# Optimization experiments

Measured on AMD Instinct MI355X. Metric: run time of the kernel, lower is better.

Reference implementation:

```python
import jax, jax.numpy as jnp
import numpy as np

B, C, H, W = 2, 64, 128, 128
HEADS, DH = 8, 32
DN = ('NCHW', 'OIHW', 'NCHW')


def _conv(x, w, pad):
    return jax.lax.conv_general_dilated(x, w, (1, 1), [(pad, pad), (pad, pad)], dimension_numbers=DN)


def _rconv3(x, w):
    # Conv3x3 module: ReflectionPad2d(1) then 3x3 VALID conv, no bias
    xp = jnp.pad(x, ((0, 0), (0, 0), (1, 1), (1, 1)), mode='reflect')
    return jax.lax.conv_general_dilated(xp, w, (1, 1), 'VALID', dimension_numbers=DN)


def _prelu(x, a):
    return jnp.where(x > 0, x, a * x)


def _l2n(x):
    # F.normalize(p=2, dim=-1), eps=1e-12
    return x / jnp.maximum(jnp.linalg.norm(x, axis=-1, keepdims=True), 1e-12)


def _ln(y, g, b):
    mu = y.mean(-1, keepdims=True)
    v = ((y - mu) ** 2).mean(-1, keepdims=True)
    return (y - mu) / jnp.sqrt(v + 1e-5) * g + b


def _qco(x, w1, sw, sb, t1w, t1b, t2w, t2b):
    # QCO_C with level_num == C
    b, Cc = x.shape[0], x.shape[1]
    L = Cc
    x1 = _rconv3(x, w1)
    x_ave = _conv(jnp.mean(x1, (2, 3), keepdims=True), sw, 0) + sb[None, :, None, None]  # [b,C,1,1]
    xq = x_ave.reshape(b, Cc)
    mn = xq.min(-1, keepdims=True)
    mx = xq.max(-1, keepdims=True)
    qs = jnp.arange(L, dtype=x.dtype)
    ql = (2.0 * qs + 1.0) / (2.0 * L) * (mx - mn) + mn  # [b,L]
    inter = (ql[:, 1] - ql[:, 0])[:, None, None]  # [b,1,1]
    quant = 1.0 - jnp.abs(ql[:, None, :] - xq[:, :, None])  # [b,C,L]
    quant = quant * (quant > 1.0 - inter)
    sta = quant.sum(1)  # [b,L]
    sta = sta / sta.sum(-1, keepdims=True)
    out = jnp.concatenate([sta[:, :, None, None], x_ave], axis=1)  # [b,2C,1,1]
    out = jax.nn.relu(_conv(out, t1w, 0) + t1b[None, :, None, None])
    out = jax.nn.relu(_conv(out, t2w, 0) + t2b[None, :, None, None])
    return out  # [b,C,1,1]


def _attention(x, w_down, w_mid, w_up, wq_l, wk_m, wv_m, wq_h, rescale,
               w_proj_l, b_proj_l, w_proj_h, b_proj_h,
               qco_w1, qco_sca_w, qco_sca_b, qco_t1_w, qco_t1_b, qco_t2_w, qco_t2_b,
               rsp_w1, rsp_prelu, rsp_w2, c31_w1, c31_prelu, c31_w2, c31_w3):
    b, Cc, Hh, Ww = x.shape
    n = Hh * Ww
    # QKV conv projections (Conv2d, zero pad 1, no bias)
    xCL = jnp.moveaxis(_conv(x, w_down, 1), 1, -1)  # [b,h,w,C]
    xCM = jnp.moveaxis(_conv(x, w_mid, 1), 1, -1)   # [b,h,w,2C]
    xCH = jnp.moveaxis(_conv(x, w_up, 1), 1, -1)    # [b,h,w,3C]
    xL = xCL.reshape(b, n, Cc)
    xM = xCM.reshape(b, n, 2 * Cc)
    xH = xCH.reshape(b, n, 3 * Cc)

    def to_heads(t, d):  # [b,n,heads*d] -> [b,heads,d,n]
        return t.reshape(b, n, HEADS, d).transpose(0, 2, 3, 1)

    q_l = _l2n(to_heads(xL @ wq_l.T, DH))            # [b,heads,DH,n]
    k_m = _l2n(to_heads(xM @ wk_m.T, 2 * DH))        # [b,heads,2DH,n]
    v_m = to_heads(xM @ wv_m.T, 2 * DH)              # [b,heads,2DH,n]
    q_h = _l2n(to_heads(xH @ wq_h.T, 3 * DH))        # [b,heads,3DH,n]

    attn_l = jax.nn.softmax(jnp.einsum('bhdn,bhen->bhde', q_l, k_m) * rescale, axis=-1)  # [b,heads,DH,2DH]
    attn_h = jax.nn.softmax(jnp.einsum('bhdn,bhen->bhde', q_h, k_m) * rescale, axis=-1)  # [b,heads,3DH,2DH]

    x_l = jnp.einsum('bhde,bhen->bhdn', attn_l, v_m).transpose(0, 3, 1, 2).reshape(b, n, HEADS * DH)
    x_h = jnp.einsum('bhde,bhen->bhdn', attn_h, v_m).transpose(0, 3, 1, 2).reshape(b, n, HEADS * 3 * DH)
    # NOTE: torch code does .view(b, c, h, w) on [b, n, c] output -> raw memory reinterpretation,
    # which is exactly jnp.reshape here (faithful to the original, including this quirk).
    out_cl = (x_l @ w_proj_l.T + b_proj_l).reshape(b, Cc, Hh, Ww)
    out_ch = (x_h @ w_proj_h.T + b_proj_h).reshape(b, 3 * Cc, Hh, Ww)

    Hcat = jnp.concatenate([out_cl, out_ch], axis=1)  # [b,4C,h,w]
    H_out = _rconv3(_prelu(_rconv3(Hcat, rsp_w1), rsp_prelu), rsp_w2)  # ReshapeBlock -> [b,C,h,w]
    att_before = _qco(jnp.moveaxis(xCL, -1, 1), qco_w1, qco_sca_w, qco_sca_b,
                      qco_t1_w, qco_t1_b, qco_t2_w, qco_t2_b)  # [b,C,1,1]
    t = _prelu(_rconv3(H_out, c31_w1), c31_prelu)
    H_add = _conv(_rconv3(t, c31_w2), c31_w3, 0)  # Conv3_1
    return H_add + H_out * att_before


def _ff_block(z, g, bb, w1, b1, w2, b2):
    # PreNorm(LayerNorm over channel) + FeedForward(Linear, LeakyReLU(0.01), Linear)
    y = jnp.moveaxis(z, 1, -1)
    y = _ln(y, g, bb)
    y = y @ w1.T + b1
    y = jnp.where(y > 0, y, 0.01 * y)
    y = y @ w2.T + b2
    return jnp.moveaxis(y, -1, 1)


def _forward(x, w_down, w_mid, w_up, wq_l, wk_m, wv_m, wq_h, rescale,
             w_proj_l, b_proj_l, w_proj_h, b_proj_h,
             qco_w1, qco_sca_w, qco_sca_b, qco_t1_w, qco_t1_b, qco_t2_w, qco_t2_b,
             rsp_w1, rsp_prelu, rsp_w2, c31_w1, c31_prelu, c31_w2, c31_w3,
             ln1_g, ln1_b, ff1_w1, ff1_b1, ff1_w2, ff1_b2,
             ln2_g, ln2_b, ff2_w1, ff2_b1, ff2_w2, ff2_b2):
    out1 = _attention(x, w_down, w_mid, w_up, wq_l, wk_m, wv_m, wq_h, rescale,
                      w_proj_l, b_proj_l, w_proj_h, b_proj_h,
                      qco_w1, qco_sca_w, qco_sca_b, qco_t1_w, qco_t1_b, qco_t2_w, qco_t2_b,
                      rsp_w1, rsp_prelu, rsp_w2, c31_w1, c31_prelu, c31_w2, c31_w3) + x
    out2 = _ff_block(out1, ln1_g, ln1_b, ff1_w1, ff1_b1, ff1_w2, ff1_b2) + out1
    out3 = _ff_block(out2, ln2_g, ln2_b, ff2_w1, ff2_b1, ff2_w2, ff2_b2) + out1
    return out3


def setup_inputs() -> dict:
    keys = iter(jax.random.split(jax.random.key(0), 48))

    def rn(shape, s=0.05):
        return (jax.random.normal(next(keys), shape, jnp.float32) * s)

    d = {
        'x': rn((B, C, H, W), 1.0),
        'w_down': rn((C, C, 3, 3)), 'w_mid': rn((2 * C, C, 3, 3)), 'w_up': rn((3 * C, C, 3, 3)),
        'wq_l': rn((HEADS * DH, C)), 'wk_m': rn((2 * HEADS * DH, 2 * C)),
        'wv_m': rn((2 * HEADS * DH, 2 * C)), 'wq_h': rn((3 * HEADS * DH, 3 * C)),
        'rescale': jnp.ones((HEADS, 1, 1), jnp.float32),
        'w_proj_l': rn((C, HEADS * DH)), 'b_proj_l': rn((C,)),
        'w_proj_h': rn((3 * C, 3 * HEADS * DH)), 'b_proj_h': rn((3 * C,)),
        'qco_w1': rn((C, C, 3, 3)), 'qco_sca_w': rn((C, C, 1, 1)), 'qco_sca_b': rn((C,)),
        'qco_t1_w': rn((C, 2 * C, 1, 1)), 'qco_t1_b': rn((C,)),
        'qco_t2_w': rn((C, C, 1, 1)), 'qco_t2_b': rn((C,)),
        'rsp_w1': rn((C, 4 * C, 3, 3)), 'rsp_prelu': jnp.array(0.25, jnp.float32), 'rsp_w2': rn((C, C, 3, 3)),
        'c31_w1': rn((C, C, 3, 3)), 'c31_prelu': jnp.array(0.25, jnp.float32),
        'c31_w2': rn((C, C, 3, 3)), 'c31_w3': rn((C, C, 1, 1)),
        'ln1_g': jnp.ones((C,), jnp.float32), 'ln1_b': jnp.zeros((C,), jnp.float32),
        'ff1_w1': rn((C, C)), 'ff1_b1': rn((C,)), 'ff1_w2': rn((C, C)), 'ff1_b2': rn((C,)),
        'ln2_g': jnp.ones((C,), jnp.float32), 'ln2_b': jnp.zeros((C,), jnp.float32),
        'ff2_w1': rn((C, C)), 'ff2_b1': rn((C,)), 'ff2_w2': rn((C, C)), 'ff2_b2': rn((C,)),
    }
    return d


def reference(x, w_down, w_mid, w_up, wq_l, wk_m, wv_m, wq_h, rescale,
              w_proj_l, b_proj_l, w_proj_h, b_proj_h,
              qco_w1, qco_sca_w, qco_sca_b, qco_t1_w, qco_t1_b, qco_t2_w, qco_t2_b,
              rsp_w1, rsp_prelu, rsp_w2, c31_w1, c31_prelu, c31_w2, c31_w3,
              ln1_g, ln1_b, ff1_w1, ff1_b1, ff1_w2, ff1_b2,
              ln2_g, ln2_b, ff2_w1, ff2_b1, ff2_w2, ff2_b2):
    return _forward(x, w_down, w_mid, w_up, wq_l, wk_m, wv_m, wq_h, rescale,
                    w_proj_l, b_proj_l, w_proj_h, b_proj_h,
                    qco_w1, qco_sca_w, qco_sca_b, qco_t1_w, qco_t1_b, qco_t2_w, qco_t2_b,
                    rsp_w1, rsp_prelu, rsp_w2, c31_w1, c31_prelu, c31_w2, c31_w3,
                    ln1_g, ln1_b, ff1_w1, ff1_b1, ff1_w2, ff1_b2,
                    ln2_g, ln2_b, ff2_w1, ff2_b1, ff2_w2, ff2_b2)
```

## Files before the change

kernel.cpp:

```cpp
#include <hip/hip_runtime.h>
#include <hip/hip_bf16.h>
#include <stdint.h>

typedef __hip_bfloat16 bf16;
typedef __attribute__((ext_vector_type(8))) __bf16 bf8v;
typedef __attribute__((ext_vector_type(8))) short short8;
typedef __attribute__((ext_vector_type(4))) short short4v;
typedef __attribute__((ext_vector_type(4))) float f32x4;
#define DEVINL __device__ __forceinline__
#define MFMA16(a,b,c) __builtin_amdgcn_mfma_f32_16x16x32_bf16((a),(b),(c),0,0,0)

DEVINL short f2bs(float f) { bf16 h = __float2bfloat16(f); return *reinterpret_cast<short*>(&h); }
DEVINL float bs2f(short s) { bf16 h = *reinterpret_cast<bf16*>(&s); return __bfloat162float(h); }


static const size_t OFF_ZBF   = 0;
static const size_t OFF_WTQ   = 29360128;
static const size_t OFF_WTR1  = 29802496;
static const size_t OFF_WTR2  = 30097408;
static const size_t OFF_WTC1  = 30171136;
static const size_t OFF_WTF   = 30244864;
static const size_t OFF_W1T   = 30318592;
static const size_t OFF_SCAWT = 30466048;
static const size_t OFF_T1WT  = 30482432;
static const size_t OFF_T2WT  = 30515200;
static const size_t OFF_GB    = 31645696;
static const size_t OFF_WQLB  = 32235520;
static const size_t OFF_WKMB  = 32268288;
static const size_t OFF_WQHB  = 32399360;
static const size_t OFF_T1    = 41082880;
static const size_t OFF_UL    = 41345024;
static const size_t OFF_UK    = 41476096;
static const size_t OFF_T1H   = 42000384;
static const size_t OFF_UH    = 42786816;
static const size_t OFF_NORMS = 43966464;
static const size_t OFF_ATTL  = 43978752;
static const size_t OFF_ATTH  = 44109824;
static const size_t OFF_WEL   = 44503040;
static const size_t OFF_WEH   = 44765184;
static const size_t OFF_ACATB = 45813760;
static const size_t OFF_TSUM  = 45944832;
static const size_t OFF_ATTB  = 45949440;
static const size_t OFF_HCATB = 45949952;
static const size_t OFF_MIDB  = 62727168;
static const size_t OFF_HOUTB = 66921472;
static const size_t OFF_WFFB  = 71115776;
static const size_t OFF_GPART = 79504384;
static const size_t OFF_HCATT = 79504384;
static const size_t OFF_XT    = 98378752;
static const size_t WS_BYTES  = 102573056;

__global__ __launch_bounds__(256) void k_transp(const float* __restrict__ x,
                                                short* __restrict__ xt) {
  __shared__ short sT[64][72];
  const int t = threadIdx.x, b = blockIdx.z, p0 = blockIdx.x * 64;
  for (int i = t; i < 1024; i += 256) {
    int c = i >> 4, p4 = (i & 15) * 4;
    float4 g = *(const float4*)&x[(((size_t)(b * 64 + c)) << 14) + p0 + p4];
    sT[p4 + 0][c] = f2bs(g.x);
    sT[p4 + 1][c] = f2bs(g.y);
    sT[p4 + 2][c] = f2bs(g.z);
    sT[p4 + 3][c] = f2bs(g.w);
  }
  __syncthreads();
  for (int i = t; i < 512; i += 256) {
    int p = i >> 3, co = (i & 7) * 8;
    *(short8*)&xt[((((size_t)b << 14) + p0 + p)) * 64 + co] = *(short8*)&sT[p][co];
  }
}

__global__ __launch_bounds__(256) void k_transph(const short* __restrict__ hc,
                                                 short* __restrict__ ht) {
  __shared__ short sT[64][72];
  const int t = threadIdx.x, b = blockIdx.z, p0 = blockIdx.x * 64, c0 = blockIdx.y * 64;
  for (int i = t; i < 512; i += 256) {
    int c = i >> 3, qo = (i & 7) * 8;
    short8 v = *(const short8*)&hc[(((size_t)(b * 256 + c0 + c)) << 14) + p0 + qo];
#pragma unroll
    for (int u = 0; u < 8; u++) sT[qo + u][c] = v[u];
  }
  __syncthreads();
  for (int i = t; i < 512; i += 256) {
    int q = i >> 3, co = (i & 7) * 8;
    *(short8*)&ht[((size_t)(b * 16384 + p0 + q)) * 256 + c0 + co] = *(short8*)&sT[q][co];
  }
}

__global__ void k_prep_all(const float* __restrict__ wd, const float* __restrict__ wm,
                           const float* __restrict__ wu, const float* __restrict__ rw1,
                           const float* __restrict__ rw2, const float* __restrict__ cw1,
                           const float* __restrict__ wql, const float* __restrict__ wkm,
                           const float* __restrict__ wqh,
                           const float* __restrict__ c31w3, const float* __restrict__ c31w2,
                           const float* __restrict__ qw1, const float* __restrict__ qscaw,
                           const float* __restrict__ qt1w, const float* __restrict__ qt2w,
                           const float* __restrict__ f11, const float* __restrict__ f12,
                           const float* __restrict__ f21, const float* __restrict__ f22,
                           bf16* __restrict__ wtq, bf16* __restrict__ wtr1,
                           bf16* __restrict__ wtr2, bf16* __restrict__ wtc1,
                           bf16* __restrict__ wqlb, bf16* __restrict__ wkmb,
                           bf16* __restrict__ wqhb, bf16* __restrict__ wtf,
                           float* __restrict__ w1t, float* __restrict__ scawt,
                           float* __restrict__ t1wt, float* __restrict__ t2wt,
                           bf16* __restrict__ wffb) {
  int i = blockIdx.x * 256 + threadIdx.x;
  if (i < 221184) {
    int tap = i / 24576, r = i % 24576, oc = r >> 6, ic = r & 63;
    float v;
    if (oc < 64)       v = wd[(oc * 64 + ic) * 9 + tap];
    else if (oc < 192) v = wm[((oc - 64) * 64 + ic) * 9 + tap];
    else               v = wu[((oc - 192) * 64 + ic) * 9 + tap];
    wtq[i] = __float2bfloat16(v);
  } else if (i < 368640) {
    int j = i - 221184;
    int tap = j / 16384, r = j % 16384, oc = r >> 8, ic = r & 255;
    wtr1[j] = __float2bfloat16(rw1[(oc * 256 + ic) * 9 + tap]);
  } else if (i < 405504) {
    int j = i - 368640;
    int tap = j / 4096, r = j % 4096, oc = r >> 6, ic = r & 63;
    wtr2[j] = __float2bfloat16(rw2[(oc * 64 + ic) * 9 + tap]);
// ... 26 lines not shown
    int o = i - 749568;
    int c = o & 63, jj = o >> 6;
    t1wt[o] = qt1w[c * 128 + jj];
  } else if (i < 761856) {
    int o = i - 757760;
    int c = o & 63, jj = o >> 6;
    t2wt[o] = qt2w[c * 64 + jj];
  } else if (i < 778240) {
    int j = i - 761856;
    int stage = j >> 12, r = j & 4095;
    const float* src = (stage == 0) ? f11 : (stage == 1) ? f12 : (stage == 2) ? f21 : f22;
    wffb[j] = __float2bfloat16(src[r]);
  }
}

__global__ __launch_bounds__(256) void k_convq(
    const short* __restrict__ xt, const short* __restrict__ wtq,
    bf16* __restrict__ zbf)
{
  __shared__ short sX[3][130][72];
  const int t = threadIdx.x, lane = t & 63, wv = t >> 6;
  const int y = blockIdx.x, ocg = blockIdx.y, b = blockIdx.z;

  for (int i = t; i < 3120; i += 256) {
    int ko = i & 7, c2 = i >> 3, col = c2 % 130, row = c2 / 130;
    int gy = y + row - 1, gx = col - 1;
    short8 vv;
    if ((gy >= 0) & (gy < 128) & (gx >= 0) & (gx < 128)) {
      vv = *(const short8*)&xt[((size_t)b * 1048576 + (size_t)((gy << 7) + gx) * 64) + ko * 8];
    } else {
// ... 310 lines not shown
  float* gp = Gp + ((size_t)(kc * 2 + b)) * 147456;
#pragma unroll
  for (int m = 0; m < 2; m++)
#pragma unroll
    for (int n = 0; n < 2; n++)
#pragma unroll
      for (int r = 0; r < 4; r++) {
        const int row = ti * 64 + wo * 32 + m * 16 + ((lane >> 4) << 2) + r;
        const int col = tj * 64 + wp * 32 + n * 16 + (lane & 15);
        float v = acc[m][n][r];
        gp[(size_t)row * 384 + col] = v;
        if (ti != tj) gp[(size_t)col * 384 + row] = v;
      }
}

__global__ void k_gredb(const float* __restrict__ Gp, bf16* __restrict__ Gb) {
  int i = blockIdx.x * 256 + threadIdx.x;
  if (i >= 294912) return;
  int b = i / 147456, e = i % 147456;
  float s = 0.f;
#pragma unroll
  for (int c = 0; c < 16; c++) s += Gp[(size_t)(c * 2 + b) * 147456 + e];
  Gb[(size_t)b * 147456 + e] = __float2bfloat16(s);
}

struct MJobs5 {
  const short* A[5];
  float* C[5];
  int lda[5], K[5], r0[5], c0[5], ldc[5];
  long sC[5];
  int nx[5], b0[6];
};

__global__ __launch_bounds__(256) void k_mgemm5(MJobs5 J, const short* __restrict__ Gb) {
  const int bx = blockIdx.x, z = blockIdx.y;
  int j = 0;
  while (bx >= J.b0[j + 1]) j++;
  const int local = bx - J.b0[j];
// ... 95 lines not shown
  const float* Bp = J.B[j] + (size_t)z * J.sB[j];
  const int K = J.K[j], lda = J.lda[j];
  const int m = y * 16 + ty, n = x * 16 + tx;
  float acc = 0.f;
  for (int k0 = 0; k0 < K; k0 += 16) {
    sa[ty][tx] = Ap[(size_t)m * lda + k0 + tx];
    sb[ty][tx] = Bp[(size_t)(k0 + ty) * 128 + n];
    __syncthreads();
#pragma unroll
    for (int kk = 0; kk < 16; kk++) acc = fmaf(sa[ty][kk], sb[kk][tx], acc);
    __syncthreads();
  }
  Cb[(size_t)z * 32768 + J.co[j] + (size_t)m * 128 + n] = __float2bfloat16(acc);
}

__global__ __launch_bounds__(256) void k_norms2(
    const float* __restrict__ UL, const float* __restrict__ UK,
    const float* __restrict__ UH,
    const float* __restrict__ wql, const float* __restrict__ wkm,
    const float* __restrict__ wqh, float* __restrict__ norms) {
  const int t = threadIdx.x, lane = t & 63;
  const int row = blockIdx.x * 4 + (t >> 6);
  const int b = row >= 1536 ? 1 : 0;
  const int r = row - b * 1536;
  const float* u; const float* wv; int K;
  if (r < 256)      { K = 64;  u = UL + (size_t)(b * 256 + r) * 64;          wv = wql + (size_t)r * 64; }
  else if (r < 768) { int e = r - 256; K = 128; u = UK + (size_t)(b * 512 + e) * 128; wv = wkm + (size_t)e * 128; }
  else              { int d = r - 768; K = 192; u = UH + (size_t)(b * 768 + d) * 192; wv = wqh + (size_t)d * 192; }
  float s = 0.f;
  for (int k = lane; k < K; k += 64) s = fmaf(u[k], wv[k], s);
#pragma unroll
  for (int o = 32; o; o >>= 1) s += __shfl_xor(s, o);
  if (lane == 0) norms[b * 1536 + r] = fmaxf(sqrtf(fmaxf(s, 0.f)), 1e-12f);
}

__global__ __launch_bounds__(256) void k_attn(
    const float* __restrict__ T1, const float* __restrict__ T1H,
    const float* __restrict__ wkm, const float* __restrict__ norms,
    const float* __restrict__ rescale,
    float* __restrict__ attL, float* __restrict__ attH)
{
  const int h = blockIdx.x, cy = blockIdx.y, b = blockIdx.z;
  const int t = threadIdx.x;
  __shared__ float sK[64 * 129];
  __shared__ float sQ[32 * 129];
  __shared__ float sNk[64];
  const int isL = (cy == 0);
  const int rbase = isL ? 0 : (cy - 1) * 32;
  const float* TQ = isL ? (T1 + (size_t)(b * 256 + h * 32) * 128)
                        : (T1H + (size_t)(b * 768 + h * 96 + rbase) * 128);
  for (int idx = t; idx < 8192; idx += 256) {
    int e = idx >> 7, k = idx & 127;
    sK[e * 129 + k] = wkm[(size_t)(h * 64 + e) * 128 + k];
  }
  for (int idx = t; idx < 4096; idx += 256) {
    int r = idx >> 7, k = idx & 127;
    sQ[r * 129 + k] = TQ[(size_t)r * 128 + k];
  }
  if (t < 64) sNk[t] = norms[b * 1536 + 256 + h * 64 + t];
  __syncthreads();

  const int w = t >> 6, lane = t & 63;
  const float rs = rescale[h];
  for (int r = w; r < 32; r += 4) {
    float s = 0.f;
    for (int k = 0; k < 128; k++) s = fmaf(sQ[r * 129 + k], sK[lane * 129 + k], s);
    float nq = norms[b * 1536 + (isL ? (h * 32 + r) : (768 + h * 96 + rbase + r))];
    float logit = s / (nq * sNk[lane]) * rs;
    float m = logit;
#pragma unroll
    for (int o = 32; o; o >>= 1) m = fmaxf(m, __shfl_xor(m, o));
    float p = __expf(logit - m);
    float den = p;
#pragma unroll
    for (int o = 32; o; o >>= 1) den += __shfl_xor(den, o);
    float av = p / den;
    if (isL) attL[((size_t)(b * 8 + h) * 32 + r) * 64 + lane] = av;
    else     attH[((size_t)(b * 8 + h) * 96 + rbase + r) * 64 + lane] = av;
  }
}

__global__ __launch_bounds__(256) void k_weff(
    const float* __restrict__ attL, const float* __restrict__ attH,
    const float* __restrict__ wvm,
    float* __restrict__ WeL, float* __restrict__ WeH)
{
  const int h = blockIdx.x, br = blockIdx.y, b = blockIdx.z;
  const int M = br ? 96 : 32;
  __shared__ float sAt[96 * 64];
  __shared__ float sV[64 * 132];
  const int t = threadIdx.x;
  const float* asrc = br ? attH + (size_t)(b * 8 + h) * 96 * 64
                         : attL + (size_t)(b * 8 + h) * 32 * 64;
  for (int idx = t; idx < M * 64; idx += 256) sAt[idx] = asrc[idx];
  for (int idx = t; idx < 8192; idx += 256) {
    int e = idx >> 7, k = idx & 127;
    sV[e * 132 + k] = wvm[(size_t)(h * 64 + e) * 128 + k];
  }
  __syncthreads();
  const int jg = t & 31, rw = t >> 5;
  float* dst = br ? WeH + (size_t)(b * 768 + h * 96) * 128
                  : WeL + (size_t)(b * 256 + h * 32) * 128;
  for (int r = rw; r < M; r += 8) {
    float4 acc = make_float4(0.f, 0.f, 0.f, 0.f);
    for (int e = 0; e < 64; e++) {
      float a = sAt[r * 64 + e];
      float4 v4 = *(const float4*)&sV[e * 132 + jg * 4];
      acc.x = fmaf(a, v4.x, acc.x);
      acc.y = fmaf(a, v4.y, acc.y);
      acc.z = fmaf(a, v4.z, acc.z);
      acc.w = fmaf(a, v4.w, acc.w);
    }
    *(float4*)&dst[(size_t)r * 128 + jg * 4] = acc;
  }
}

__global__ __launch_bounds__(256) void k_tsum2(const bf16* __restrict__ Z,
                                               float* __restrict__ Tsum) {
  const int c = blockIdx.x & 63, b = blockIdx.x >> 6;
  const bf16* src = Z + (((size_t)(b * 384 + c)) << 14);
  const int t = threadIdx.x;
  __shared__ float sc[16];
  __shared__ float red[4][9];
  float a9[9] = {};
  for (int i = t; i < 2048; i += 256) {
    int y = i >> 4, x0 = (i & 15) * 8;
    short8 v8 = *(const short8*)&src[(y << 7) + x0];
    float vs[8], s8 = 0.f;
#pragma unroll
    for (int u = 0; u < 8; u++) { vs[u] = bs2f(v8[u]); s8 += vs[u]; }
    a9[0] += s8;
    int ri = (y == 0) ? 0 : (y == 1) ? 1 : (y == 126) ? 2 : (y == 127) ? 3 : -1;
    if (ri >= 0) a9[1 + ri] += s8;
    if (x0 == 0)   { a9[5] += vs[0]; a9[6] += vs[1]; }
    if (x0 == 120) { a9[7] += vs[6]; a9[8] += vs[7]; }
    if (ri >= 0) {
      if (x0 == 0)   { sc[ri * 4 + 0] = vs[0]; sc[ri * 4 + 1] = vs[1]; }
      if (x0 == 120) { sc[ri * 4 + 2] = vs[6]; sc[ri * 4 + 3] = vs[7]; }
    }
  }
#pragma unroll
  for (int q = 0; q < 9; q++)
#pragma unroll
    for (int o = 32; o; o >>= 1) a9[q] += __shfl_xor(a9[q], o);
  const int w = t >> 6;
  if ((t & 63) == 0)
#pragma unroll
    for (int q = 0; q < 9; q++) red[w][q] = a9[q];
  __syncthreads();
  if (t == 0) {
    float s9[9];
#pragma unroll
    for (int q = 0; q < 9; q++) s9[q] = red[0][q] + red[1][q] + red[2][q] + red[3][q];
    const float T = s9[0];
    float R[4] = {s9[1], s9[2], s9[3], s9[4]};
    const float C0 = s9[5], C1 = s9[6], C126 = s9[7], C127 = s9[8];
    float rs[4][3];
#pragma unroll
    for (int ri = 0; ri < 4; ri++) {
      rs[ri][0] = R[ri] - sc[ri * 4 + 3] + sc[ri * 4 + 1];
      rs[ri][1] = R[ri];
      rs[ri][2] = R[ri] - sc[ri * 4 + 0] + sc[ri * 4 + 2];
    }
    float A3[3] = {T - C127 + C1, T, T - C0 + C126};
#pragma unroll
    for (int dx = 0; dx < 3; dx++) {
      Tsum[blockIdx.x * 9 + 0 * 3 + dx] = A3[dx] - rs[3][dx] + rs[1][dx];
      Tsum[blockIdx.x * 9 + 1 * 3 + dx] = A3[dx];
      Tsum[blockIdx.x * 9 + 2 * 3 + dx] = A3[dx] - rs[0][dx] + rs[2][dx];
    }
  }
}

__global__ __launch_bounds__(64) void k_qco(
    const float* __restrict__ Tsum, const float* __restrict__ w1t,
    const float* __restrict__ scawt, const float* __restrict__ scab,
    const float* __restrict__ t1wt, const float* __restrict__ t1b,
    const float* __restrict__ t2wt, const float* __restrict__ t2b,
    float* __restrict__ attb)
{
  const int b = blockIdx.x, c = threadIdx.x;
  __shared__ float sm[64], sxq[64], scat[128], sh1[64];
  float acc = 0.f;
  for (int j = 0; j < 64; j++) {
#pragma unroll
    for (int tap = 0; tap < 9; tap++)
      acc = fmaf(w1t[((j * 9 + tap) << 6) + c], Tsum[(b * 64 + j) * 9 + tap], acc);
  }
  sm[c] = acc * (1.f / 16384.f);
  __syncthreads();
  float xa = scab[c];
  for (int j = 0; j < 64; j++) xa = fmaf(scawt[(j << 6) + c], sm[j], xa);
  sxq[c] = xa;
  __syncthreads();
  float mn = xa, mx = xa;
#pragma unroll
  for (int o = 32; o; o >>= 1) {
    mn = fminf(mn, __shfl_xor(mn, o));
    mx = fmaxf(mx, __shfl_xor(mx, o));
  }
  float inter = (mx - mn) * (1.f / 64.f);
  float ql = (2.f * c + 1.f) / 128.f * (mx - mn) + mn;
  float sta = 0.f;
  for (int j = 0; j < 64; j++) {
    float q = 1.f - fabsf(ql - sxq[j]);
    sta += (q > 1.f - inter) ? q : 0.f;
  }
  float tot = sta;
#pragma unroll
  for (int o = 32; o; o >>= 1) tot += __shfl_xor(tot, o);
  sta = sta / fmaxf(tot, 1e-30f);
  scat[c] = sta; scat[64 + c] = xa;
  __syncthreads();
  float h = t1b[c];
  for (int j = 0; j < 128; j++) h = fmaf(t1wt[(j << 6) + c], scat[j], h);
  h = fmaxf(h, 0.f);
  sh1[c] = h;
  __syncthreads();
  float o2 = t2b[c];
  for (int j = 0; j < 64; j++) o2 = fmaf(t2wt[(j << 6) + c], sh1[j], o2);
  attb[b * 64 + c] = fmaxf(o2, 0.f);
}

extern "C" void kernel_launch(void* const* d_in, const int* in_sizes, int n_in,
                              void* d_out, int out_size, void* d_ws, size_t ws_size,
                              hipStream_t stream)
{
  if (ws_size < WS_BYTES) return;
  char* ws = (char*)d_ws;

  const float* x       = (const float*)d_in[0];
  const float* w_down  = (const float*)d_in[1];
  const float* w_mid   = (const float*)d_in[2];
  const float* w_up    = (const float*)d_in[3];
  const float* wq_l    = (const float*)d_in[4];
  const float* wk_m    = (const float*)d_in[5];
// ... 40 lines not shown
  float* w1t   = (float*)(ws + OFF_W1T);
  float* scawt = (float*)(ws + OFF_SCAWT);
  float* t1wt  = (float*)(ws + OFF_T1WT);
  float* t2wt  = (float*)(ws + OFF_T2WT);
  bf16*  Gb    = (bf16*)(ws + OFF_GB);
  bf16*  wqlb  = (bf16*)(ws + OFF_WQLB);
  bf16*  wkmb  = (bf16*)(ws + OFF_WKMB);
  bf16*  wqhb  = (bf16*)(ws + OFF_WQHB);
  float* gpart = (float*)(ws + OFF_GPART);
  float* T1    = (float*)(ws + OFF_T1);
  float* UL    = (float*)(ws + OFF_UL);
  float* UK    = (float*)(ws + OFF_UK);
  float* T1H   = (float*)(ws + OFF_T1H);
  float* UH    = (float*)(ws + OFF_UH);
  float* norms = (float*)(ws + OFF_NORMS);
  float* attL  = (float*)(ws + OFF_ATTL);
  float* attH  = (float*)(ws + OFF_ATTH);
  float* WeL   = (float*)(ws + OFF_WEL);
  float* WeH   = (float*)(ws + OFF_WEH);
  bf16*  acatb = (bf16*)(ws + OFF_ACATB);
  float* tsum  = (float*)(ws + OFF_TSUM);
  float* attb  = (float*)(ws + OFF_ATTB);
  bf16*  hcatb = (bf16*)(ws + OFF_HCATB);
  short* hcatT = (short*)(ws + OFF_HCATT);
  short* midb  = (short*)(ws + OFF_MIDB);
  short* houtb = (short*)(ws + OFF_HOUTB);
  bf16*  wffb  = (bf16*)(ws + OFF_WFFB);
  short* xt    = (short*)(ws + OFF_XT);

  k_transp<<<dim3(256, 1, 2), 256, 0, stream>>>(x, xt);
  k_prep_all<<<dim3(3040), 256, 0, stream>>>(
      w_down, w_mid, w_up, rsp_w1, rsp_w2, c31_w1, wq_l, wk_m, wq_h,
      c31_w3, c31_w2, qco_w1, qsca_w, qt1_w, qt2_w,
      ff1_w1, ff1_w2, ff2_w1, ff2_w2,
      wtq, wtr1, wtr2, wtc1, wqlb, wkmb, wqhb, wtf,
      w1t, scawt, t1wt, t2wt, wffb);

  k_convq<<<dim3(128, 2, 2), 256, 0, stream>>>(xt, (const short*)wtq, zbf);

  k_gramm<<<dim3(21, 16, 2), 256, 0, stream>>>((const short*)zbf, gpart);
  k_gredb<<<dim3(1152), 256, 0, stream>>>(gpart, Gb);

  k_tsum2<<<dim3(128), 256, 0, stream>>>(zbf, tsum);

  MJobs5 M5;
  M5.A[0] = (const short*)wqlb; M5.lda[0] = 64;  M5.K[0] = 64;  M5.r0[0] = 0;   M5.c0[0] = 64;  M5.C[0] = T1;  M5.ldc[0] = 128; M5.sC[0] = 32768;  M5.nx[0] = 2;
  M5.A[1] = (const short*)wqlb; M5.lda[1] = 64;  M5.K[1] = 64;  M5.r0[1] = 0;   M5.c0[1] = 0;   M5.C[1] = UL;  M5.ldc[1] = 64;  M5.sC[1] = 16384;  M5.nx[1] = 1;
  M5.A[2] = (const short*)wkmb; M5.lda[2] = 128; M5.K[2] = 128; M5.r0[2] = 64;  M5.c0[2] = 64;  M5.C[2] = UK;  M5.ldc[2] = 128; M5.sC[2] = 65536;  M5.nx[2] = 2;
  M5.A[3] = (const short*)wqhb; M5.lda[3] = 192; M5.K[3] = 192; M5.r0[3] = 192; M5.c0[3] = 64;  M5.C[3] = T1H; M5.ldc[3] = 128; M5.sC[3] = 98304;  M5.nx[3] = 2;
  M5.A[4] = (const short*)wqhb; M5.lda[4] = 192; M5.K[4] = 192; M5.r0[4] = 192; M5.c0[4] = 192; M5.C[4] = UH;  M5.ldc[4] = 192; M5.sC[4] = 147456; M5.nx[4] = 3;
  M5.b0[0] = 0; M5.b0[1] = 8; M5.b0[2] = 12; M5.b0[3] = 28; M5.b0[4] = 52; M5.b0[5] = 88;
  k_mgemm5<<<dim3(88, 2), 256, 0, stream>>>(M5, (const short*)Gb);

  k_norms2<<<dim3(768), 256, 0, stream>>>(UL, UK, UH, wq_l, wk_m, wq_h, norms);
  k_qco<<<dim3(2), 64, 0, stream>>>(tsum, w1t, scawt, qsca_b, t1wt, qt1_b, t2wt, qt2_b, attb);
  k_attn<<<dim3(8, 4, 2), 256, 0, stream>>>(T1, T1H, wk_m, norms, rescale, attL, attH);
  k_weff<<<dim3(8, 2, 2), 256, 0, stream>>>(attL, attH, wv_m, WeL, WeH);

  Jobs2 J2;
  J2.A[0] = w_proj_l; J2.B[0] = WeL; J2.K[0] = 256; J2.lda[0] = 256; J2.sB[0] = 32768; J2.nx[0] = 8; J2.co[0] = 0;
  J2.A[1] = w_proj_h; J2.B[1] = WeH; J2.K[1] = 768; J2.lda[1] = 768; J2.sB[1] = 98304; J2.nx[1] = 8; J2.co[1] = 8192;
  J2.b0[0] = 0; J2.b0[1] = 32; J2.b0[2] = 128;
  k_sgemm2b<<<dim3(128, 2), 256, 0, stream>>>(J2, acatb);

  k_pixm<<<dim3(256, 4, 2), 256, 0, stream>>>((const short*)zbf, (const short*)acatb,
                                              b_proj_l, b_proj_h, hcatb);

  k_transph<<<dim3(256, 4, 2), 256, 0, stream>>>((const short*)hcatb, hcatT);

  k_conv64<1><<<dim3(128, 2, 2), 256, 0, stream>>>(
      hcatT, 256, 4194304L, 256, (const short*)wtr1, midb, rsp_pr);
  k_conv64<0><<<dim3(128, 2, 2), 256, 0, stream>>>(
// ... 11 lines not shown
```

Before: 271.5 us.

## Merge small independent kernels and fuse attention softmax with value-weight product

Folds the input transpose into the weight-prep launch and the Gram reduction and tile-sum into one launch (`k_gt`). It also puts the norms and QCO head in one launch (`k_nq`) and fuses attention logits/softmax with the effective-weight product in `k_attw`, keeping attention probabilities in shared memory. This removes several kernel launches and the global round trip for attL/attH. The trade-off is that the fused attention kernel runs only 16 blocks, handling both branches serially with large shared-memory use, so there is less parallelism for that stage.

```diff
diff --git a/kernel.cpp b/kernel.cpp
--- a/kernel.cpp
+++ b/kernel.cpp
@@ -34,8 +34,6 @@
 static const size_t OFF_T1H   = 42000384;
 static const size_t OFF_UH    = 42786816;
 static const size_t OFF_NORMS = 43966464;
-static const size_t OFF_ATTL  = 43978752;
-static const size_t OFF_ATTH  = 44109824;
 static const size_t OFF_WEL   = 44503040;
 static const size_t OFF_WEH   = 44765184;
 static const size_t OFF_ACATB = 45813760;
@@ -50,60 +48,46 @@
 static const size_t OFF_XT    = 98378752;
 static const size_t WS_BYTES  = 102573056;
 
-__global__ __launch_bounds__(256) void k_transp(const float* __restrict__ x,
-                                                short* __restrict__ xt) {
+__global__ __launch_bounds__(256) void k_prep_all(
+    const float* __restrict__ wd, const float* __restrict__ wm,
+    const float* __restrict__ wu, const float* __restrict__ rw1,
+    const float* __restrict__ rw2, const float* __restrict__ cw1,
+    const float* __restrict__ wql, const float* __restrict__ wkm,
+    const float* __restrict__ wqh,
+    const float* __restrict__ c31w3, const float* __restrict__ c31w2,
+    const float* __restrict__ qw1, const float* __restrict__ qscaw,
+    const float* __restrict__ qt1w, const float* __restrict__ qt2w,
+    const float* __restrict__ f11, const float* __restrict__ f12,
+    const float* __restrict__ f21, const float* __restrict__ f22,
+    const float* __restrict__ x,
+    bf16* __restrict__ wtq, bf16* __restrict__ wtr1,
+    bf16* __restrict__ wtr2, bf16* __restrict__ wtc1,
+    bf16* __restrict__ wqlb, bf16* __restrict__ wkmb,
+    bf16* __restrict__ wqhb, bf16* __restrict__ wtf,
+    float* __restrict__ w1t, float* __restrict__ scawt,
+    float* __restrict__ t1wt, float* __restrict__ t2wt,
+    bf16* __restrict__ wffb, short* __restrict__ xt) {
   __shared__ short sT[64][72];
-  const int t = threadIdx.x, b = blockIdx.z, p0 = blockIdx.x * 64;
-  for (int i = t; i < 1024; i += 256) {
-    int c = i >> 4, p4 = (i & 15) * 4;
-    float4 g = *(const float4*)&x[(((size_t)(b * 64 + c)) << 14) + p0 + p4];
-    sT[p4 + 0][c] = f2bs(g.x);
-    sT[p4 + 1][c] = f2bs(g.y);
-    sT[p4 + 2][c] = f2bs(g.z);
-    sT[p4 + 3][c] = f2bs(g.w);
-  }
-  __syncthreads();
-  for (int i = t; i < 512; i += 256) {
-    int p = i >> 3, co = (i & 7) * 8;
-    *(short8*)&xt[((((size_t)b << 14) + p0 + p)) * 64 + co] = *(short8*)&sT[p][co];
-  }
-}
-
-__global__ __launch_bounds__(256) void k_transph(const short* __restrict__ hc,
-                                                 short* __restrict__ ht) {
-  __shared__ short sT[64][72];
-  const int t = threadIdx.x, b = blockIdx.z, p0 = blockIdx.x * 64, c0 = blockIdx.y * 64;
-  for (int i = t; i < 512; i += 256) {
-    int c = i >> 3, qo = (i & 7) * 8;
-    short8 v = *(const short8*)&hc[(((size_t)(b * 256 + c0 + c)) << 14) + p0 + qo];
-#pragma unroll
-    for (int u = 0; u < 8; u++) sT[qo + u][c] = v[u];
-  }
-  __syncthreads();
-  for (int i = t; i < 512; i += 256) {
-    int q = i >> 3, co = (i & 7) * 8;
-    *(short8*)&ht[((size_t)(b * 16384 + p0 + q)) * 256 + c0 + co] = *(short8*)&sT[q][co];
-  }
-}
-
-__global__ void k_prep_all(const float* __restrict__ wd, const float* __restrict__ wm,
-                           const float* __restrict__ wu, const float* __restrict__ rw1,
-                           const float* __restrict__ rw2, const float* __restrict__ cw1,
-                           const float* __restrict__ wql, const float* __restrict__ wkm,
-                           const float* __restrict__ wqh,
-                           const float* __restrict__ c31w3, const float* __restrict__ c31w2,
-                           const float* __restrict__ qw1, const float* __restrict__ qscaw,
-                           const float* __restrict__ qt1w, const float* __restrict__ qt2w,
-                           const float* __restrict__ f11, const float* __restrict__ f12,
-                           const float* __restrict__ f21, const float* __restrict__ f22,
-                           bf16* __restrict__ wtq, bf16* __restrict__ wtr1,
-                           bf16* __restrict__ wtr2, bf16* __restrict__ wtc1,
-                           bf16* __restrict__ wqlb, bf16* __restrict__ wkmb,
-                           bf16* __restrict__ wqhb, bf16* __restrict__ wtf,
-                           float* __restrict__ w1t, float* __restrict__ scawt,
-                           float* __restrict__ t1wt, float* __restrict__ t2wt,
-                           bf16* __restrict__ wffb) {
-  int i = blockIdx.x * 256 + threadIdx.x;
+  const int t = threadIdx.x;
+  if (blockIdx.x >= 3040) {
+    const int j = blockIdx.x - 3040;
+    const int b = j >> 8, p0 = (j & 255) * 64;
+    for (int i = t; i < 1024; i += 256) {
+      int c = i >> 4, p4 = (i & 15) * 4;
+      float4 g = *(const float4*)&x[(((size_t)(b * 64 + c)) << 14) + p0 + p4];
+      sT[p4 + 0][c] = f2bs(g.x);
+      sT[p4 + 1][c] = f2bs(g.y);
+      sT[p4 + 2][c] = f2bs(g.z);
+      sT[p4 + 3][c] = f2bs(g.w);
+    }
+    __syncthreads();
+    for (int i = t; i < 512; i += 256) {
+      int p = i >> 3, co = (i & 7) * 8;
+      *(short8*)&xt[((((size_t)b << 14) + p0 + p)) * 64 + co] = *(short8*)&sT[p][co];
+    }
+    return;
+  }
+  int i = blockIdx.x * 256 + t;
   if (i < 221184) {
     int tap = i / 24576, r = i % 24576, oc = r >> 6, ic = r & 63;
     float v;
@@ -160,6 +144,23 @@
   }
 }
 
+__global__ __launch_bounds__(256) void k_transph(const short* __restrict__ hc,
+                                                 short* __restrict__ ht) {
+  __shared__ short sT[64][72];
+  const int t = threadIdx.x, b = blockIdx.z, p0 = blockIdx.x * 64, c0 = blockIdx.y * 64;
+  for (int i = t; i < 512; i += 256) {
+    int c = i >> 3, qo = (i & 7) * 8;
+    short8 v = *(const short8*)&hc[(((size_t)(b * 256 + c0 + c)) << 14) + p0 + qo];
+#pragma unroll
+    for (int u = 0; u < 8; u++) sT[qo + u][c] = v[u];
+  }
+  __syncthreads();
+  for (int i = t; i < 512; i += 256) {
+    int q = i >> 3, co = (i & 7) * 8;
+    *(short8*)&ht[((size_t)(b * 16384 + p0 + q)) * 256 + c0 + co] = *(short8*)&sT[q][co];
+  }
+}
+
 __global__ __launch_bounds__(256) void k_convq(
     const short* __restrict__ xt, const short* __restrict__ wtq,
     bf16* __restrict__ zbf)
@@ -500,14 +501,74 @@
       }
 }
 
-__global__ void k_gredb(const float* __restrict__ Gp, bf16* __restrict__ Gb) {
-  int i = blockIdx.x * 256 + threadIdx.x;
-  if (i >= 294912) return;
-  int b = i / 147456, e = i % 147456;
-  float s = 0.f;
-#pragma unroll
-  for (int c = 0; c < 16; c++) s += Gp[(size_t)(c * 2 + b) * 147456 + e];
-  Gb[(size_t)b * 147456 + e] = __float2bfloat16(s);
+__global__ __launch_bounds__(256) void k_gt(const float* __restrict__ Gp,
+                                            bf16* __restrict__ Gb,
+                                            const bf16* __restrict__ Z,
+                                            float* __restrict__ Tsum) {
+  __shared__ float sc[16];
+  __shared__ float red[4][9];
+  const int t = threadIdx.x;
+  if (blockIdx.x < 1152) {
+    int i = blockIdx.x * 256 + t;
+    if (i >= 294912) return;
+    int b = i / 147456, e = i % 147456;
+    float s = 0.f;
+#pragma unroll
+    for (int c = 0; c < 16; c++) s += Gp[(size_t)(c * 2 + b) * 147456 + e];
+    Gb[(size_t)b * 147456 + e] = __float2bfloat16(s);
+    return;
+  }
+  const int bid = blockIdx.x - 1152;
+  const int c = bid & 63, b = bid >> 6;
+  const bf16* src = Z + (((size_t)(b * 384 + c)) << 14);
+  float a9[9] = {};
+  for (int i = t; i < 2048; i += 256) {
+    int y = i >> 4, x0 = (i & 15) * 8;
+    short8 v8 = *(const short8*)&src[(y << 7) + x0];
+    float vs[8], s8 = 0.f;
+#pragma unroll
+    for (int u = 0; u < 8; u++) { vs[u] = bs2f(v8[u]); s8 += vs[u]; }
+    a9[0] += s8;
+    int ri = (y == 0) ? 0 : (y == 1) ? 1 : (y == 126) ? 2 : (y == 127) ? 3 : -1;
+    if (ri >= 0) a9[1 + ri] += s8;
+    if (x0 == 0)   { a9[5] += vs[0]; a9[6] += vs[1]; }
+    if (x0 == 120) { a9[7] += vs[6]; a9[8] += vs[7]; }
+    if (ri >= 0) {
+      if (x0 == 0)   { sc[ri * 4 + 0] = vs[0]; sc[ri * 4 + 1] = vs[1]; }
+      if (x0 == 120) { sc[ri * 4 + 2] = vs[6]; sc[ri * 4 + 3] = vs[7]; }
+    }
+  }
+#pragma unroll
+  for (int q = 0; q < 9; q++)
+#pragma unroll
+    for (int o = 32; o; o >>= 1) a9[q] += __shfl_xor(a9[q], o);
+  const int w = t >> 6;
+  if ((t & 63) == 0)
+#pragma unroll
+    for (int q = 0; q < 9; q++) red[w][q] = a9[q];
+  __syncthreads();
+  if (t == 0) {
+    float s9[9];
+#pragma unroll
+    for (int q = 0; q < 9; q++) s9[q] = red[0][q] + red[1][q] + red[2][q] + red[3][q];
+    const float T = s9[0];
+    float R[4] = {s9[1], s9[2], s9[3], s9[4]};
+    const float C0 = s9[5], C1 = s9[6], C126 = s9[7], C127 = s9[8];
+    float rs[4][3];
+#pragma unroll
+    for (int ri = 0; ri < 4; ri++) {
+      rs[ri][0] = R[ri] - sc[ri * 4 + 3] + sc[ri * 4 + 1];
+      rs[ri][1] = R[ri];
+      rs[ri][2] = R[ri] - sc[ri * 4 + 0] + sc[ri * 4 + 2];
+    }
+    float A3[3] = {T - C127 + C1, T, T - C0 + C126};
+#pragma unroll
+    for (int dx = 0; dx < 3; dx++) {
+      Tsum[bid * 9 + 0 * 3 + dx] = A3[dx] - rs[3][dx] + rs[1][dx];
+      Tsum[bid * 9 + 1 * 3 + dx] = A3[dx];
+      Tsum[bid * 9 + 2 * 3 + dx] = A3[dx] - rs[0][dx] + rs[2][dx];
+    }
+  }
 }
 
 struct MJobs5 {
@@ -633,212 +694,150 @@
   Cb[(size_t)z * 32768 + J.co[j] + (size_t)m * 128 + n] = __float2bfloat16(acc);
 }
 
-__global__ __launch_bounds__(256) void k_norms2(
+__global__ __launch_bounds__(256) void k_nq(
     const float* __restrict__ UL, const float* __restrict__ UK,
     const float* __restrict__ UH,
     const float* __restrict__ wql, const float* __restrict__ wkm,
-    const float* __restrict__ wqh, float* __restrict__ norms) {
-  const int t = threadIdx.x, lane = t & 63;
-  const int row = blockIdx.x * 4 + (t >> 6);
-  const int b = row >= 1536 ? 1 : 0;
-  const int r = row - b * 1536;
-  const float* u; const float* wv; int K;
-  if (r < 256)      { K = 64;  u = UL + (size_t)(b * 256 + r) * 64;          wv = wql + (size_t)r * 64; }
-  else if (r < 768) { int e = r - 256; K = 128; u = UK + (size_t)(b * 512 + e) * 128; wv = wkm + (size_t)e * 128; }
-  else              { int d = r - 768; K = 192; u = UH + (size_t)(b * 768 + d) * 192; wv = wqh + (size_t)d * 192; }
-  float s = 0.f;
-  for (int k = lane; k < K; k += 64) s = fmaf(u[k], wv[k], s);
-#pragma unroll
-  for (int o = 32; o; o >>= 1) s += __shfl_xor(s, o);
-  if (lane == 0) norms[b * 1536 + r] = fmaxf(sqrtf(fmaxf(s, 0.f)), 1e-12f);
-}
-
-__global__ __launch_bounds__(256) void k_attn(
-    const float* __restrict__ T1, const float* __restrict__ T1H,
-    const float* __restrict__ wkm, const float* __restrict__ norms,
-    const float* __restrict__ rescale,
-    float* __restrict__ attL, float* __restrict__ attH)
-{
-  const int h = blockIdx.x, cy = blockIdx.y, b = blockIdx.z;
-  const int t = threadIdx.x;
-  __shared__ float sK[64 * 129];
-  __shared__ float sQ[32 * 129];
-  __shared__ float sNk[64];
-  const int isL = (cy == 0);
-  const int rbase = isL ? 0 : (cy - 1) * 32;
-  const float* TQ = isL ? (T1 + (size_t)(b * 256 + h * 32) * 128)
-                        : (T1H + (size_t)(b * 768 + h * 96 + rbase) * 128);
-  for (int idx = t; idx < 8192; idx += 256) {
-    int e = idx >> 7, k = idx & 127;
-    sK[e * 129 + k] = wkm[(size_t)(h * 64 + e) * 128 + k];
-  }
-  for (int idx = t; idx < 4096; idx += 256) {
-    int r = idx >> 7, k = idx & 127;
-    sQ[r * 129 + k] = TQ[(size_t)r * 128 + k];
-  }
-  if (t < 64) sNk[t] = norms[b * 1536 + 256 + h * 64 + t];
-  __syncthreads();
-
-  const int w = t >> 6, lane = t & 63;
-  const float rs = rescale[h];
-  for (int r = w; r < 32; r += 4) {
-    float s = 0.f;
-    for (int k = 0; k < 128; k++) s = fmaf(sQ[r * 129 + k], sK[lane * 129 + k], s);
-    float nq = norms[b * 1536 + (isL ? (h * 32 + r) : (768 + h * 96 + rbase + r))];
-    float logit = s / (nq * sNk[lane]) * rs;
-    float m = logit;
-#pragma unroll
-    for (int o = 32; o; o >>= 1) m = fmaxf(m, __shfl_xor(m, o));
-    float p = __expf(logit - m);
-    float den = p;
-#pragma unroll
-    for (int o = 32; o; o >>= 1) den += __shfl_xor(den, o);
-    float av = p / den;
-    if (isL) attL[((size_t)(b * 8 + h) * 32 + r) * 64 + lane] = av;
-    else     attH[((size_t)(b * 8 + h) * 96 + rbase + r) * 64 + lane] = av;
-  }
-}
-
-__global__ __launch_bounds__(256) void k_weff(
-    const float* __restrict__ attL, const float* __restrict__ attH,
-    const float* __restrict__ wvm,
-    float* __restrict__ WeL, float* __restrict__ WeH)
-{
-  const int h = blockIdx.x, br = blockIdx.y, b = blockIdx.z;
-  const int M = br ? 96 : 32;
-  __shared__ float sAt[96 * 64];
-  __shared__ float sV[64 * 132];
-  const int t = threadIdx.x;
-  const float* asrc = br ? attH + (size_t)(b * 8 + h) * 96 * 64
-                         : attL + (size_t)(b * 8 + h) * 32 * 64;
-  for (int idx = t; idx < M * 64; idx += 256) sAt[idx] = asrc[idx];
-  for (int idx = t; idx < 8192; idx += 256) {
-    int e = idx >> 7, k = idx & 127;
-    sV[e * 132 + k] = wvm[(size_t)(h * 64 + e) * 128 + k];
-  }
-  __syncthreads();
-  const int jg = t & 31, rw = t >> 5;
-  float* dst = br ? WeH + (size_t)(b * 768 + h * 96) * 128
-                  : WeL + (size_t)(b * 256 + h * 32) * 128;
-  for (int r = rw; r < M; r += 8) {
-    float4 acc = make_float4(0.f, 0.f, 0.f, 0.f);
-    for (int e = 0; e < 64; e++) {
-      float a = sAt[r * 64 + e];
-      float4 v4 = *(const float4*)&sV[e * 132 + jg * 4];
-      acc.x = fmaf(a, v4.x, acc.x);
-      acc.y = fmaf(a, v4.y, acc.y);
-      acc.z = fmaf(a, v4.z, acc.z);
-      acc.w = fmaf(a, v4.w, acc.w);
-    }
-    *(float4*)&dst[(size_t)r * 128 + jg * 4] = acc;
-  }
-}
-
-__global__ __launch_bounds__(256) void k_tsum2(const bf16* __restrict__ Z,
-                                               float* __restrict__ Tsum) {
-  const int c = blockIdx.x & 63, b = blockIdx.x >> 6;
-  const bf16* src = Z + (((size_t)(b * 384 + c)) << 14);
-  const int t = threadIdx.x;
-  __shared__ float sc[16];
-  __shared__ float red[4][9];
-  float a9[9] = {};
-  for (int i = t; i < 2048; i += 256) {
-    int y = i >> 4, x0 = (i & 15) * 8;
-    short8 v8 = *(const short8*)&src[(y << 7) + x0];
-    float vs[8], s8 = 0.f;
-#pragma unroll
-    for (int u = 0; u < 8; u++) { vs[u] = bs2f(v8[u]); s8 += vs[u]; }
-    a9[0] += s8;
-    int ri = (y == 0) ? 0 : (y == 1) ? 1 : (y == 126) ? 2 : (y == 127) ? 3 : -1;
-    if (ri >= 0) a9[1 + ri] += s8;
-    if (x0 == 0)   { a9[5] += vs[0]; a9[6] += vs[1]; }
-    if (x0 == 120) { a9[7] += vs[6]; a9[8] += vs[7]; }
-    if (ri >= 0) {
-      if (x0 == 0)   { sc[ri * 4 + 0] = vs[0]; sc[ri * 4 + 1] = vs[1]; }
-      if (x0 == 120) { sc[ri * 4 + 2] = vs[6]; sc[ri * 4 + 3] = vs[7]; }
-    }
-  }
-#pragma unroll
-  for (int q = 0; q < 9; q++)
-#pragma unroll
-    for (int o = 32; o; o >>= 1) a9[q] += __shfl_xor(a9[q], o);
-  const int w = t >> 6;
-  if ((t & 63) == 0)
-#pragma unroll
-    for (int q = 0; q < 9; q++) red[w][q] = a9[q];
-  __syncthreads();
-  if (t == 0) {
-    float s9[9];
-#pragma unroll
-    for (int q = 0; q < 9; q++) s9[q] = red[0][q] + red[1][q] + red[2][q] + red[3][q];
-    const float T = s9[0];
-    float R[4] = {s9[1], s9[2], s9[3], s9[4]};
-    const float C0 = s9[5], C1 = s9[6], C126 = s9[7], C127 = s9[8];
-    float rs[4][3];
-#pragma unroll
-    for (int ri = 0; ri < 4; ri++) {
-      rs[ri][0] = R[ri] - sc[ri * 4 + 3] + sc[ri * 4 + 1];
-      rs[ri][1] = R[ri];
-      rs[ri][2] = R[ri] - sc[ri * 4 + 0] + sc[ri * 4 + 2];
-    }
-    float A3[3] = {T - C127 + C1, T, T - C0 + C126};
-#pragma unroll
-    for (int dx = 0; dx < 3; dx++) {
-      Tsum[blockIdx.x * 9 + 0 * 3 + dx] = A3[dx] - rs[3][dx] + rs[1][dx];
-      Tsum[blockIdx.x * 9 + 1 * 3 + dx] = A3[dx];
-      Tsum[blockIdx.x * 9 + 2 * 3 + dx] = A3[dx] - rs[0][dx] + rs[2][dx];
-    }
-  }
-}
-
-__global__ __launch_bounds__(64) void k_qco(
+    const float* __restrict__ wqh, float* __restrict__ norms,
     const float* __restrict__ Tsum, const float* __restrict__ w1t,
     const float* __restrict__ scawt, const float* __restrict__ scab,
     const float* __restrict__ t1wt, const float* __restrict__ t1b,
     const float* __restrict__ t2wt, const float* __restrict__ t2b,
     float* __restrict__ attb)
 {
-  const int b = blockIdx.x, c = threadIdx.x;
   __shared__ float sm[64], sxq[64], scat[128], sh1[64];
-  float acc = 0.f;
-  for (int j = 0; j < 64; j++) {
-#pragma unroll
-    for (int tap = 0; tap < 9; tap++)
-      acc = fmaf(w1t[((j * 9 + tap) << 6) + c], Tsum[(b * 64 + j) * 9 + tap], acc);
-  }
-  sm[c] = acc * (1.f / 16384.f);
+  const int t = threadIdx.x, lane = t & 63;
+  if (blockIdx.x < 768) {
+    const int row = blockIdx.x * 4 + (t >> 6);
+    const int b = row >= 1536 ? 1 : 0;
+    const int r = row - b * 1536;
+    const float* u; const float* wv; int K;
+    if (r < 256)      { K = 64;  u = UL + (size_t)(b * 256 + r) * 64;          wv = wql + (size_t)r * 64; }
+    else if (r < 768) { int e = r - 256; K = 128; u = UK + (size_t)(b * 512 + e) * 128; wv = wkm + (size_t)e * 128; }
+    else              { int d = r - 768; K = 192; u = UH + (size_t)(b * 768 + d) * 192; wv = wqh + (size_t)d * 192; }
+    float s = 0.f;
+    for (int k = lane; k < K; k += 64) s = fmaf(u[k], wv[k], s);
+#pragma unroll
+    for (int o = 32; o; o >>= 1) s += __shfl_xor(s, o);
+    if (lane == 0) norms[b * 1536 + r] = fmaxf(sqrtf(fmaxf(s, 0.f)), 1e-12f);
+    return;
+  }
+  const int b = blockIdx.x - 768, c = t;
+  if (t < 64) {
+    float acc = 0.f;
+    for (int j = 0; j < 64; j++) {
+#pragma unroll
+      for (int tap = 0; tap < 9; tap++)
+        acc = fmaf(w1t[((j * 9 + tap) << 6) + c], Tsum[(b * 64 + j) * 9 + tap], acc);
+    }
+    sm[c] = acc * (1.f / 16384.f);
+  }
   __syncthreads();
-  float xa = scab[c];
-  for (int j = 0; j < 64; j++) xa = fmaf(scawt[(j << 6) + c], sm[j], xa);
-  sxq[c] = xa;
+  if (t < 64) {
+    float xa = scab[c];
+    for (int j = 0; j < 64; j++) xa = fmaf(scawt[(j << 6) + c], sm[j], xa);
+    sxq[c] = xa;
+  }
   __syncthreads();
-  float mn = xa, mx = xa;
-#pragma unroll
-  for (int o = 32; o; o >>= 1) {
-    mn = fminf(mn, __shfl_xor(mn, o));
-    mx = fmaxf(mx, __shfl_xor(mx, o));
-  }
-  float inter = (mx - mn) * (1.f / 64.f);
-  float ql = (2.f * c + 1.f) / 128.f * (mx - mn) + mn;
-  float sta = 0.f;
-  for (int j = 0; j < 64; j++) {
-    float q = 1.f - fabsf(ql - sxq[j]);
-    sta += (q > 1.f - inter) ? q : 0.f;
-  }
-  float tot = sta;
-#pragma unroll
-  for (int o = 32; o; o >>= 1) tot += __shfl_xor(tot, o);
-  sta = sta / fmaxf(tot, 1e-30f);
-  scat[c] = sta; scat[64 + c] = xa;
+  if (t < 64) {
+    float xa = sxq[c];
+    float mn = xa, mx = xa;
+#pragma unroll
+    for (int o = 32; o; o >>= 1) {
+      mn = fminf(mn, __shfl_xor(mn, o));
+      mx = fmaxf(mx, __shfl_xor(mx, o));
+    }
+    float inter = (mx - mn) * (1.f / 64.f);
+    float ql = (2.f * c + 1.f) / 128.f * (mx - mn) + mn;
+    float sta = 0.f;
+    for (int j = 0; j < 64; j++) {
+      float q = 1.f - fabsf(ql - sxq[j]);
+      sta += (q > 1.f - inter) ? q : 0.f;
+    }
+    float tot = sta;
+#pragma unroll
+    for (int o = 32; o; o >>= 1) tot += __shfl_xor(tot, o);
+    sta = sta / fmaxf(tot, 1e-30f);
+    scat[c] = sta; scat[64 + c] = xa;
+  }
   __syncthreads();
-  float h = t1b[c];
-  for (int j = 0; j < 128; j++) h = fmaf(t1wt[(j << 6) + c], scat[j], h);
-  h = fmaxf(h, 0.f);
-  sh1[c] = h;
+  if (t < 64) {
+    float h = t1b[c];
+    for (int j = 0; j < 128; j++) h = fmaf(t1wt[(j << 6) + c], scat[j], h);
+    h = fmaxf(h, 0.f);
+    sh1[c] = h;
+  }
   __syncthreads();
-  float o2 = t2b[c];
-  for (int j = 0; j < 64; j++) o2 = fmaf(t2wt[(j << 6) + c], sh1[j], o2);
-  attb[b * 64 + c] = fmaxf(o2, 0.f);
+  if (t < 64) {
+    float o2 = t2b[c];
+    for (int j = 0; j < 64; j++) o2 = fmaf(t2wt[(j << 6) + c], sh1[j], o2);
+    attb[b * 64 + c] = fmaxf(o2, 0.f);
+  }
+}
+
+__global__ __launch_bounds__(256) void k_attw(
+    const float* __restrict__ T1, const float* __restrict__ T1H,
+    const float* __restrict__ wkm, const float* __restrict__ wvm,
+    const float* __restrict__ norms, const float* __restrict__ rescale,
+    float* __restrict__ WeL, float* __restrict__ WeH)
+{
+  const int h = blockIdx.x, b = blockIdx.y;
+  __shared__ float sK[64 * 129];
+  __shared__ float sV[64 * 132];
+  __shared__ float sQ[96 * 129];
+  __shared__ float sAt[96 * 64];
+  __shared__ float sNk[64];
+  const int t = threadIdx.x;
+  for (int idx = t; idx < 8192; idx += 256) {
+    int e = idx >> 7, k = idx & 127;
+    sK[e * 129 + k] = wkm[(size_t)(h * 64 + e) * 128 + k];
+    sV[e * 132 + k] = wvm[(size_t)(h * 64 + e) * 128 + k];
+  }
+  if (t < 64) sNk[t] = norms[b * 1536 + 256 + h * 64 + t];
+
+  const float rs = rescale[h];
+  for (int br = 0; br < 2; br++) {
+    const int M = br ? 96 : 32;
+    const float* TQ = br ? (T1H + (size_t)(b * 768 + h * 96) * 128)
+                         : (T1 + (size_t)(b * 256 + h * 32) * 128);
+    for (int idx = t; idx < M * 128; idx += 256) {
+      int r = idx >> 7, k = idx & 127;
+      sQ[r * 129 + k] = TQ[(size_t)r * 128 + k];
+    }
+    __syncthreads();
+    const int w = t >> 6, lane = t & 63;
+    for (int r = w; r < M; r += 4) {
+      float s = 0.f;
+      for (int k = 0; k < 128; k++) s = fmaf(sQ[r * 129 + k], sK[lane * 129 + k], s);
+      float nq = norms[b * 1536 + (br ? (768 + h * 96 + r) : (h * 32 + r))];
+      float logit = s / (nq * sNk[lane]) * rs;
+      float m = logit;
+#pragma unroll
+      for (int o = 32; o; o >>= 1) m = fmaxf(m, __shfl_xor(m, o));
+      float p = __expf(logit - m);
+      float den = p;
+#pragma unroll
+      for (int o = 32; o; o >>= 1) den += __shfl_xor(den, o);
+      sAt[r * 64 + lane] = p / den;
+    }
+    __syncthreads();
+    const int jg = t & 31, rw = t >> 5;
+    float* dst = br ? WeH + (size_t)(b * 768 + h * 96) * 128
+                    : WeL + (size_t)(b * 256 + h * 32) * 128;
+    for (int r = rw; r < M; r += 8) {
+      float4 acc = make_float4(0.f, 0.f, 0.f, 0.f);
+      for (int e = 0; e < 64; e++) {
+        float a = sAt[r * 64 + e];
+        float4 v4 = *(const float4*)&sV[e * 132 + jg * 4];
+        acc.x = fmaf(a, v4.x, acc.x);
+        acc.y = fmaf(a, v4.y, acc.y);
+        acc.z = fmaf(a, v4.z, acc.z);
+        acc.w = fmaf(a, v4.w, acc.w);
+      }
+      *(float4*)&dst[(size_t)r * 128 + jg * 4] = acc;
+    }
+    __syncthreads();
+  }
 }
 
 extern "C" void kernel_launch(void* const* d_in, const int* in_sizes, int n_in,
@@ -909,8 +908,6 @@
   float* T1H   = (float*)(ws + OFF_T1H);
   float* UH    = (float*)(ws + OFF_UH);
   float* norms = (float*)(ws + OFF_NORMS);
-  float* attL  = (float*)(ws + OFF_ATTL);
-  float* attH  = (float*)(ws + OFF_ATTH);
   float* WeL   = (float*)(ws + OFF_WEL);
   float* WeH   = (float*)(ws + OFF_WEH);
   bf16*  acatb = (bf16*)(ws + OFF_ACATB);
@@ -923,20 +920,18 @@
   bf16*  wffb  = (bf16*)(ws + OFF_WFFB);
   short* xt    = (short*)(ws + OFF_XT);
 
-  k_transp<<<dim3(256, 1, 2), 256, 0, stream>>>(x, xt);
-  k_prep_all<<<dim3(3040), 256, 0, stream>>>(
+  k_prep_all<<<dim3(3552), 256, 0, stream>>>(
       w_down, w_mid, w_up, rsp_w1, rsp_w2, c31_w1, wq_l, wk_m, wq_h,
       c31_w3, c31_w2, qco_w1, qsca_w, qt1_w, qt2_w,
-      ff1_w1, ff1_w2, ff2_w1, ff2_w2,
+      ff1_w1, ff1_w2, ff2_w1, ff2_w2, x,
       wtq, wtr1, wtr2, wtc1, wqlb, wkmb, wqhb, wtf,
-      w1t, scawt, t1wt, t2wt, wffb);
+      w1t, scawt, t1wt, t2wt, wffb, xt);
 
   k_convq<<<dim3(128, 2, 2), 256, 0, stream>>>(xt, (const short*)wtq, zbf);
 
   k_gramm<<<dim3(21, 16, 2), 256, 0, stream>>>((const short*)zbf, gpart);
-  k_gredb<<<dim3(1152), 256, 0, stream>>>(gpart, Gb);
-
-  k_tsum2<<<dim3(128), 256, 0, stream>>>(zbf, tsum);
+
+  k_gt<<<dim3(1280), 256, 0, stream>>>(gpart, Gb, zbf, tsum);
 
   MJobs5 M5;
   M5.A[0] = (const short*)wqlb; M5.lda[0] = 64;  M5.K[0] = 64;  M5.r0[0] = 0;   M5.c0[0] = 64;  M5.C[0] = T1;  M5.ldc[0] = 128; M5.sC[0] = 32768;  M5.nx[0] = 2;
@@ -947,10 +942,10 @@
   M5.b0[0] = 0; M5.b0[1] = 8; M5.b0[2] = 12; M5.b0[3] = 28; M5.b0[4] = 52; M5.b0[5] = 88;
   k_mgemm5<<<dim3(88, 2), 256, 0, stream>>>(M5, (const short*)Gb);
 
-  k_norms2<<<dim3(768), 256, 0, stream>>>(UL, UK, UH, wq_l, wk_m, wq_h, norms);
-  k_qco<<<dim3(2), 64, 0, stream>>>(tsum, w1t, scawt, qsca_b, t1wt, qt1_b, t2wt, qt2_b, attb);
-  k_attn<<<dim3(8, 4, 2), 256, 0, stream>>>(T1, T1H, wk_m, norms, rescale, attL, attH);
-  k_weff<<<dim3(8, 2, 2), 256, 0, stream>>>(attL, attH, wv_m, WeL, WeH);
+  k_nq<<<dim3(770), 256, 0, stream>>>(UL, UK, UH, wq_l, wk_m, wq_h, norms,
+                                      tsum, w1t, scawt, qsca_b, t1wt, qt1_b, t2wt, qt2_b, attb);
+
+  k_attw<<<dim3(8, 2), 256, 0, stream>>>(T1, T1H, wk_m, wv_m, norms, rescale, WeL, WeH);
 
   Jobs2 J2;
   J2.A[0] = w_proj_l; J2.B[0] = WeL; J2.K[0] = 256; J2.lda[0] = 256; J2.sB[0] = 32768; J2.nx[0] = 8; J2.co[0] = 0;
```

After: 305.1 us. 12.4% more time.
